# Kernel optimization log

Hardware: AMD Instinct MI355X
Metric: run time of the kernel (lower is better)

Reference implementation:

```python
import jax, jax.numpy as jnp
import numpy as np

COMMA_ID = 1010   # BERT wordpiece id for ','
H, NH, HD = 768, 8, 96
B, S = 64, 512
NSEG = 17         # 16 commas per row -> 17 segments
EPS = 1e-5


def setup_inputs() -> dict:
    key = jax.random.key(0)
    ks = jax.random.split(key, 16)
    text_hs = jax.random.normal(ks[0], (B, S, H), jnp.float32)
    cols_hs = jax.random.normal(ks[1], (B, S, H), jnp.float32)
    ids = jax.random.randint(ks[2], (B, S), 0, 30522)
    ids = jnp.where(ids == COMMA_ID, COMMA_ID + 1, ids)  # avoid accidental commas
    comma_pos = jnp.arange(16, 257, 16)                  # 16 commas per row
    ids = ids.at[:, comma_pos].set(COMMA_ID)
    sc = 0.02
    wq = jax.random.normal(ks[3], (H, H), jnp.float32) * sc
    wk = jax.random.normal(ks[4], (H, H), jnp.float32) * sc
    wv = jax.random.normal(ks[5], (H, H), jnp.float32) * sc
    bq = jnp.zeros((H,), jnp.float32)
    bk = jnp.zeros((H,), jnp.float32)
    bv = jnp.zeros((H,), jnp.float32)
    wo = jax.random.normal(ks[6], (H, H), jnp.float32) * sc
    bo = jnp.zeros((H,), jnp.float32)
    gamma = jnp.ones((H,), jnp.float32)
    beta = jnp.zeros((H,), jnp.float32)
    w_out = jax.random.normal(ks[7], (1, H), jnp.float32) * sc
    b_out = jnp.zeros((1,), jnp.float32)
    return dict(text_hs=text_hs, cols_hs=cols_hs, wq=wq, wk=wk, wv=wv,
                bq=bq, bk=bk, bv=bv, wo=wo, bo=bo, gamma=gamma, beta=beta,
                w_out=w_out, b_out=b_out, columns_input_ids=ids, n_segments=NSEG)


def _forward(text_hs, cols_hs, wq, wk, wv, bq, bk, bv, wo, bo,
             gamma, beta, w_out, b_out, columns_input_ids, n_segments):
    t = text_hs[:, 1:, :]   # drop first token, as in forward()  [B, L, H]
    c = cols_hs[:, 1:, :]
    L = t.shape[1]
    # --- nn.MultiheadAttention(query=cols, key=value=text), batch_first ---
    q = c @ wq.T + bq
    k = t @ wk.T + bk
    v = t @ wv.T + bv
    split = lambda x: x.reshape(x.shape[0], -1, NH, HD).transpose(0, 2, 1, 3)
    scores = jnp.einsum('bhqd,bhkd->bhqk', split(q), split(k)) / np.sqrt(HD).astype(np.float32)
    attn = jax.nn.softmax(scores, axis=-1)
    ctx = jnp.einsum('bhqk,bhkd->bhqd', attn, split(v))
    ctx = ctx.transpose(0, 2, 1, 3).reshape(c.shape[0], L, H)
    attn_out = ctx @ wo.T + bo
    # --- BatchNorm1d over channels (training-mode batch stats) ---
    xt = attn_out.transpose(0, 2, 1)            # [B, H, L]
    mu = xt.mean(axis=(0, 2), keepdims=True)
    var = xt.var(axis=(0, 2), keepdims=True)     # biased, as torch BN normalization
    xn = (xt - mu) / jnp.sqrt(var + EPS) * gamma[None, :, None] + beta[None, :, None]
    cross_out = c + xn.transpose(0, 2, 1)       # residual add
    fv = (cross_out @ w_out.T + b_out).squeeze(-1)   # [B, L] scores per token
    # --- compose_outputs: mean-pool comma-delimited ragged spans ---
    is_comma = columns_input_ids[:, :L] == COMMA_ID
    seg = jnp.cumsum(is_comma.astype(jnp.int32), axis=1) - is_comma.astype(jnp.int32)
    mask = (jnp.arange(L)[None, :] >= 1) & (~is_comma)    # slice_start=1, commas excluded
    oh = ((seg[:, :, None] == jnp.arange(n_segments)[None, None, :])
          & mask[:, :, None]).astype(fv.dtype)            # [B, L, J]
    sums = jnp.einsum('blj,bl->bj', oh, fv)
    cnt = oh.sum(axis=1)
    return sums / jnp.maximum(cnt, 1.0)                   # [B, n_segments]


def reference(text_hs, cols_hs, wq, wk, wv, bq, bk, bv, wo, bo,
              gamma, beta, w_out, b_out, columns_input_ids, n_segments):
    return _forward(text_hs, cols_hs, wq, wk, wv, bq, bk, bv, wo, bo,
                    gamma, beta, w_out, b_out, columns_input_ids, n_segments)
```

## Files before the change

kernel.cpp:

```cpp
#include <hip/hip_runtime.h>
#include <hip/hip_bf16.h>

#define COMMA_IDC 1010
#define NHEAD 8
#define Ll 511
#define Mrows 32704
#define NSEG 17

typedef __attribute__((ext_vector_type(8))) short bf16x8;
typedef __attribute__((ext_vector_type(4))) float f32x4;
typedef unsigned short u16;
typedef unsigned int u32;
typedef unsigned long long u64;

__device__ __forceinline__ u16 f2b(float f) {
  __hip_bfloat16 h = __float2bfloat16(f);
  return *reinterpret_cast<u16*>(&h);
}
__device__ __forceinline__ float b2f(u16 u) {
  u32 x = ((u32)u) << 16;
  return __builtin_bit_cast(float, x);
}

__device__ __forceinline__ void gld_lds16(const void* g, void* l) {
  __builtin_amdgcn_global_load_lds(
      (const __attribute__((address_space(1))) void*)(u64)g,
      (__attribute__((address_space(3))) void*)(u32)(u64)l,
      16, 0, 0);
}

#define MFMA16(a, b, c) __builtin_amdgcn_mfma_f32_16x16x32_bf16(a, b, c, 0, 0, 0)
#define LGKM0 do { asm volatile("s_waitcnt lgkmcnt(0)" ::: "memory"); __builtin_amdgcn_sched_barrier(0); } while (0)
#define VMC(n) asm volatile("s_waitcnt vmcnt(" #n ")" ::: "memory")

__global__ void conv_sliced2(const float4* __restrict__ s0, const float4* __restrict__ s1,
                             ushort4* __restrict__ d0, ushort4* __restrict__ d1) {
  const float4* src = blockIdx.z ? s1 : s0;
  ushort4* dst = blockIdx.z ? d1 : d0;
  int b = blockIdx.y;
  int idx = blockIdx.x * 256 + threadIdx.x;
  if (idx >= Ll * 192) return;
  int l = idx / 192, c = idx - l * 192;
  float4 v = src[(b * 512 + l + 1) * 192 + c];
  ushort4 o; o.x = f2b(v.x); o.y = f2b(v.y); o.z = f2b(v.z); o.w = f2b(v.w);
  dst[(b * Ll + l) * 192 + c] = o;
}

__global__ void conv_w(const float4* __restrict__ wq, const float4* __restrict__ wk,
                       const float4* __restrict__ wv, const float4* __restrict__ wo,
                       ushort4* __restrict__ wqkvb, ushort4* __restrict__ wob) {
  int i = blockIdx.x * 256 + threadIdx.x;
  int seg = i / 147456, off = i - seg * 147456;
  const float4* s = (seg == 0) ? wq : ((seg == 1) ? wk : ((seg == 2) ? wv : wo));
  ushort4* d = (seg == 3) ? wob : (wqkvb + seg * 147456);
  float4 v = s[off];
  ushort4 o; o.x = f2b(v.x); o.y = f2b(v.y); o.z = f2b(v.z); o.w = f2b(v.w);
  d[off] = o;
}

__global__ void zero_kernel(float* p, int n) {
  int i = blockIdx.x * 256 + threadIdx.x;
  if (i < n) p[i] = 0.f;
}

#define LDA8(db, i, kk) (*(const bf16x8*)(sMem + (db) + ((i) * 32 + wr * 16 + fr) * 64 + ((((kk) * 4 + fq) ^ xm) << 3)))
#define LDW8(db, j, kk) (*(const bf16x8*)(sMem + (db) + 16384 + ((j) * 64 + wc * 16 + fr) * 64 + ((((kk) * 4 + fq) ^ xm) << 3)))

template<int NTILES, int NOUT, int QNT, bool DO_STATS>
__global__ __launch_bounds__(512, 2) void gemm256(
    const u16* __restrict__ A0, const u16* __restrict__ A1, const u16* __restrict__ W,
    const float* __restrict__ b0, const float* __restrict__ b1, const float* __restrict__ b2,
    u16* __restrict__ outp, float* __restrict__ ssum, float* __restrict__ ssq)
{
  __shared__ __align__(16) u16 sMem[65536];
  const int tid = threadIdx.x;
  const int lane = tid & 63, wid = tid >> 6;
  const int fr = lane & 15, fq = lane >> 4;
  const int wr = wid >> 2, wc = wid & 3;
  const int xm = fr & 7;

  int fid = blockIdx.x;
  int xcd = fid & 7, w = fid >> 3;
  int mrow = xcd * 16 + w / NTILES;
  int ncol = w - (w / NTILES) * NTILES;
  const int m0 = mrow * 256, n0 = ncol * 256;
  const u16* __restrict__ A = (ncol < QNT) ? A0 : A1;

  const int rS = tid >> 3;
  const int cS = (tid & 7) ^ (rS & 7);
  const u16* gA0 = A + (u64)(m0 + rS) * 768 + cS * 8;
  const u16* gW0 = W + (u64)(n0 + rS) * 768 + cS * 8;
  const u32 st0 = tid * 8;

  auto stALO = [&](u32 db, int kb) {
    gld_lds16(gA0 + kb, sMem + db + st0);
    gld_lds16(gA0 + kb + 49152, sMem + db + st0 + 4096);
  };
  auto stWLO = [&](u32 db, int kb) {
    gld_lds16(gW0 + kb, sMem + db + 16384 + st0);
    gld_lds16(gW0 + kb + 49152, sMem + db + 16384 + st0 + 4096);
  };
  auto stAHI = [&](u32 db, int kb) {
    gld_lds16(gA0 + kb + 98304, sMem + db + 8192 + st0);
    gld_lds16(gA0 + kb + 147456, sMem + db + 8192 + st0 + 4096);
  };
  auto stWHI = [&](u32 db, int kb) {
    gld_lds16(gW0 + kb + 98304, sMem + db + 24576 + st0);
    gld_lds16(gW0 + kb + 147456, sMem + db + 24576 + st0 + 4096);
  };

  f32x4 acc[8][4] = {};
  bf16x8 af[4][2], wl[2][2], wh[2][2];

  stALO(0, 0); stWLO(0, 0); stAHI(0, 0); stWHI(0, 0);
  VMC(4);
  __builtin_amdgcn_s_barrier();

#pragma unroll 1
  for (int kt = 0; kt < 11; ++kt) {
    const u32 db = (u32)(kt & 1) * 32768;
    const u32 nb = db ^ 32768u;
    const int kb1 = (kt + 1) * 64;

#pragma unroll
    for (int i = 0; i < 4; i++) { af[i][0] = LDA8(db, i, 0); af[i][1] = LDA8(db, i, 1); }
#pragma unroll
    for (int j = 0; j < 2; j++) { wl[j][0] = LDW8(db, j, 0); wl[j][1] = LDW8(db, j, 1); }
    stALO(nb, kb1);
    __builtin_amdgcn_s_barrier();
    LGKM0;
    __builtin_amdgcn_s_setprio(1);
#pragma unroll
    for (int i = 0; i < 4; i++)
#pragma unroll
      for (int j = 0; j < 2; j++) {
        acc[i][j] = MFMA16(af[i][0], wl[j][0], acc[i][j]);
        acc[i][j] = MFMA16(af[i][1], wl[j][1], acc[i][j]);
      }
    __builtin_amdgcn_s_setprio(0);
    VMC(4);
    __builtin_amdgcn_s_barrier();

#pragma unroll
    for (int i = 0; i < 4; i++) { af[i][0] = LDA8(db, i + 4, 0); af[i][1] = LDA8(db, i + 4, 1); }
    stWLO(nb, kb1);
    __builtin_amdgcn_s_barrier();
    LGKM0;
    __builtin_amdgcn_s_setprio(1);
#pragma unroll
    for (int i = 0; i < 4; i++)
#pragma unroll
      for (int j = 0; j < 2; j++) {
        acc[i + 4][j] = MFMA16(af[i][0], wl[j][0], acc[i + 4][j]);
        acc[i + 4][j] = MFMA16(af[i][1], wl[j][1], acc[i + 4][j]);
      }
    __builtin_amdgcn_s_setprio(0);
    VMC(4);
    __builtin_amdgcn_s_barrier();

#pragma unroll
    for (int j = 0; j < 2; j++) { wh[j][0] = LDW8(db, j + 2, 0); wh[j][1] = LDW8(db, j + 2, 1); }
    stAHI(nb, kb1);
    __builtin_amdgcn_s_barrier();
    LGKM0;
    __builtin_amdgcn_s_setprio(1);
#pragma unroll
    for (int i = 0; i < 4; i++)
#pragma unroll
      for (int j = 0; j < 2; j++) {
        acc[i + 4][j + 2] = MFMA16(af[i][0], wh[j][0], acc[i + 4][j + 2]);
        acc[i + 4][j + 2] = MFMA16(af[i][1], wh[j][1], acc[i + 4][j + 2]);
      }
    __builtin_amdgcn_s_setprio(0);
    __builtin_amdgcn_s_barrier();

#pragma unroll
    for (int i = 0; i < 4; i++) { af[i][0] = LDA8(db, i, 0); af[i][1] = LDA8(db, i, 1); }
    stWHI(nb, kb1);
    __builtin_amdgcn_s_barrier();
    LGKM0;
    __builtin_amdgcn_s_setprio(1);
#pragma unroll
    for (int i = 0; i < 4; i++)
#pragma unroll
      for (int j = 0; j < 2; j++) {
        acc[i][j + 2] = MFMA16(af[i][0], wh[j][0], acc[i][j + 2]);
        acc[i][j + 2] = MFMA16(af[i][1], wh[j][1], acc[i][j + 2]);
      }
    __builtin_amdgcn_s_setprio(0);
    VMC(4);
    __builtin_amdgcn_s_barrier();
  }

  {
    const u32 db = 32768u;
#pragma unroll
    for (int i = 0; i < 4; i++) { af[i][0] = LDA8(db, i, 0); af[i][1] = LDA8(db, i, 1); }
#pragma unroll
    for (int j = 0; j < 2; j++) { wl[j][0] = LDW8(db, j, 0); wl[j][1] = LDW8(db, j, 1); }
    __builtin_amdgcn_s_barrier();
    LGKM0;
#pragma unroll
    for (int i = 0; i < 4; i++)
#pragma unroll
      for (int j = 0; j < 2; j++) {
        acc[i][j] = MFMA16(af[i][0], wl[j][0], acc[i][j]);
        acc[i][j] = MFMA16(af[i][1], wl[j][1], acc[i][j]);
      }
    VMC(2);
    __builtin_amdgcn_s_barrier();
#pragma unroll
    for (int i = 0; i < 4; i++) { af[i][0] = LDA8(db, i + 4, 0); af[i][1] = LDA8(db, i + 4, 1); }
    __builtin_amdgcn_s_barrier();
    LGKM0;
#pragma unroll
    for (int i = 0; i < 4; i++)
#pragma unroll
      for (int j = 0; j < 2; j++) {
        acc[i + 4][j] = MFMA16(af[i][0], wl[j][0], acc[i + 4][j]);
        acc[i + 4][j] = MFMA16(af[i][1], wl[j][1], acc[i + 4][j]);
      }
    VMC(0);
    __builtin_amdgcn_s_barrier();
#pragma unroll
    for (int j = 0; j < 2; j++) { wh[j][0] = LDW8(db, j + 2, 0); wh[j][1] = LDW8(db, j + 2, 1); }
    LGKM0;
#pragma unroll
    for (int i = 0; i < 4; i++)
#pragma unroll
      for (int j = 0; j < 2; j++) {
        acc[i + 4][j + 2] = MFMA16(af[i][0], wh[j][0], acc[i + 4][j + 2]);
        acc[i + 4][j + 2] = MFMA16(af[i][1], wh[j][1], acc[i + 4][j + 2]);
      }
#pragma unroll
    for (int i = 0; i < 4; i++) { af[i][0] = LDA8(db, i, 0); af[i][1] = LDA8(db, i, 1); }
    LGKM0;
#pragma unroll
    for (int i = 0; i < 4; i++)
#pragma unroll
      for (int j = 0; j < 2; j++) {
        acc[i][j + 2] = MFMA16(af[i][0], wh[j][0], acc[i][j + 2]);
        acc[i][j + 2] = MFMA16(af[i][1], wh[j][1], acc[i][j + 2]);
      }
  }

  const float* bp = (n0 < 768) ? b0 : ((n0 < 1536) ? b1 : b2);
  const int bcol = n0 % 768;
  float bj[4];
#pragma unroll
  for (int j = 0; j < 4; j++) bj[j] = bp[bcol + j * 64 + wc * 16 + fr];

  if constexpr (DO_STATS) {
#pragma unroll
    for (int j = 0; j < 4; j++) {
      float s = 0.f, q = 0.f;
#pragma unroll
      for (int i = 0; i < 8; i++)
#pragma unroll
        for (int r = 0; r < 4; r++) {
          int m = m0 + i * 32 + wr * 16 + fq * 4 + r;
          float v = acc[i][j][r] + bj[j];
          if (m < Mrows) { s += v; q += v * v; }
        }
      s += __shfl_xor(s, 16, 64); s += __shfl_xor(s, 32, 64);
      q += __shfl_xor(q, 16, 64); q += __shfl_xor(q, 32, 64);
      if (fq == 0) {
        int col = n0 + j * 64 + wc * 16 + fr;
        atomicAdd(&ssum[col], s);
        atomicAdd(&ssq[col], q);
      }
    }
  }

#pragma unroll
  for (int h = 0; h < 2; h++) {
    __syncthreads();
#pragma unroll
    for (int i2 = 0; i2 < 4; i2++) {
      int i = h * 4 + i2;
#pragma unroll
      for (int j = 0; j < 4; j++)
#pragma unroll
        for (int r = 0; r < 4; r++)
          sMem[(i2 * 32 + wr * 16 + fq * 4 + r) * 264 + j * 64 + wc * 16 + fr] =
              f2b(acc[i][j][r] + bj[j]);
    }
    __syncthreads();
#pragma unroll
    for (int it = 0; it < 8; it++) {
      int chunk = tid + it * 512;
      int lr = chunk >> 5, ch = chunk & 31;
      *(bf16x8*)(outp + (u64)(m0 + h * 128 + lr) * NOUT + n0 + ch * 8) =
          *(const bf16x8*)(sMem + lr * 264 + ch * 8);
    }
  }
}

__global__ __launch_bounds__(256) void vtrans(const u16* __restrict__ QKV, u16* __restrict__ VT) {
  __shared__ __align__(16) u16 sT[128 * 128];
  int bh = blockIdx.y;
  int b = bh >> 3, h = bh & 7;
  int l0 = blockIdx.x * 128;
  u16* outp = VT + (u64)bh * 96 * 512;
  int t = threadIdx.x;
#pragma unroll
  for (int k = 0; k < 6; k++) {
    int c = t + k * 256;
    int l = c / 12, ch = c - l * 12;
    int lc = l0 + l; if (lc > 510) lc = 510;
    bf16x8 v = *(const bf16x8*)(QKV + (u64)(b * 511 + lc) * 2304 + 1536 + h * 96 + ch * 8);
    int chunk = l * 16 + (ch ^ ((l >> 3) & 7));
    *(bf16x8*)(sT + chunk * 8) = v;
  }
  __syncthreads();
#pragma unroll
  for (int k = 0; k < 6; k++) {
    int c = t + k * 256;
    int d = c >> 4, lch = c & 15;
    u16 vals[8];
#pragma unroll
    for (int k2 = 0; k2 < 8; k2++) {
      int r = lch * 8 + k2;
      int idx = r * 128 + (((d >> 3) ^ (lch & 7)) << 3) + (d & 7);
      vals[k2] = sT[idx];
    }
    bf16x8 o;
#pragma unroll
    for (int k2 = 0; k2 < 8; k2++) o[k2] = (short)vals[k2];
    *(bf16x8*)(outp + (u64)d * 512 + l0 + lch * 8) = o;
  }
}

#define PST 68
__global__ __launch_bounds__(256) void attn_kernel(
    const u16* __restrict__ QKV, const u16* __restrict__ VT, u16* __restrict__ ctxb)
{
  __shared__ __align__(16) u16 sK[64 * 96];
  __shared__ __align__(16) u16 sV[96 * 64];
  __shared__ __align__(16) u16 sP[4][16 * PST];
  const int tid = threadIdx.x, lane = tid & 63, wid = tid >> 6;
  int fid = blockIdx.x;
  int xcd = fid & 7, slot = (fid >> 3) & 3, grp = fid >> 5;
  int bh = grp * 8 + xcd;
  int b = bh >> 3, h = bh & 7;
  int q0 = slot * 128;
  const int fr = lane & 15, fq = lane >> 4;
  const u64 mb = (u64)(b * 511);
  const u64 hbV = (u64)bh * 96 * 512;

  bf16x8 qf[2][3];
#pragma unroll
  for (int sub = 0; sub < 2; sub++) {
    int qr = q0 + wid * 32 + sub * 16 + fr; if (qr > 510) qr = 510;
#pragma unroll
    for (int ks = 0; ks < 3; ks++)
      qf[sub][ks] = *(const bf16x8*)(QKV + (mb + qr) * 2304 + h * 96 + ks * 32 + fq * 8);
  }

  f32x4 ctx[2][6] = {};
  f32x4 sumP[2] = {};

  int kRow[3]; u32 kOffG[3], vOffG[3];
  u16 *kDst[3], *vDst[3];
#pragma unroll
  for (int k = 0; k < 3; k++) {
    int c = wid * 64 + lane + k * 256;
    int r = c / 12, p = c - r * 12;
    int s = p - (r % 12); if (s < 0) s += 12;
    kRow[k] = r;
    kOffG[k] = 768 + h * 96 + s * 8;
    kDst[k] = sK + (u32)(wid * 64 + k * 256) * 8;
    int d = c >> 3, pv = c & 7;
    int sv = pv ^ (d & 7);
    vOffG[k] = (u32)(d * 512 + sv * 8);
    vDst[k] = sV + (u32)(wid * 64 + k * 256) * 8;
  }

  const float cs = 0.10206207261596575f;
  u16* pw = &sP[wid][0];

  for (int kv0 = 0; kv0 < 511; kv0 += 64) {
    __syncthreads();
#pragma unroll
    for (int k = 0; k < 3; k++) {
      int row = kv0 + kRow[k]; if (row > 510) row = 510;
      gld_lds16(QKV + (mb + row) * 2304 + kOffG[k], kDst[k]);
    }
#pragma unroll
    for (int k = 0; k < 3; k++)
      gld_lds16(VT + hbV + vOffG[k] + kv0, vDst[k]);
    __syncthreads();

    bf16x8 kf[4][3];
#pragma unroll
    for (int kv16 = 0; kv16 < 4; kv16++) {
      int r = kv16 * 16 + fr;
      int rm = r % 12;
#pragma unroll
      for (int ks = 0; ks < 3; ks++) {
        int sidx = ks * 4 + fq + rm; if (sidx >= 12) sidx -= 12;
        kf[kv16][ks] = *(const bf16x8*)(sK + (r * 12 + sidx) * 8);
      }
    }

#pragma unroll
    for (int sub = 0; sub < 2; sub++) {
      f32x4 s[4] = {};
#pragma unroll
      for (int kv16 = 0; kv16 < 4; kv16++)
#pragma unroll
        for (int ks = 0; ks < 3; ks++)
          s[kv16] = MFMA16(qf[sub][ks], kf[kv16][ks], s[kv16]);

#pragma unroll
      for (int kv16 = 0; kv16 < 4; kv16++) {
        bool ok = (kv0 + kv16 * 16 + fr) < Ll;
#pragma unroll
        for (int r = 0; r < 4; r++) {
          float e = __expf(s[kv16][r] * cs);
          e = ok ? e : 0.f;
          sumP[sub][r] += e;
          pw[(fq * 4 + r) * PST + kv16 * 16 + fr] = f2b(e);
        }
      }
      bf16x8 pf0 = *(const bf16x8*)(pw + fr * PST + fq * 8);
      bf16x8 pf1 = *(const bf16x8*)(pw + fr * PST + 32 + fq * 8);
#pragma unroll
      for (int df = 0; df < 6; df++) {
        int row = df * 16 + fr;
        int xv = fr & 7;
        bf16x8 vf0 = *(const bf16x8*)(sV + row * 64 + ((fq ^ xv) << 3));
        bf16x8 vf1 = *(const bf16x8*)(sV + row * 64 + (((4 + fq) ^ xv) << 3));
        ctx[sub][df] = MFMA16(pf0, vf0, ctx[sub][df]);
        ctx[sub][df] = MFMA16(pf1, vf1, ctx[sub][df]);
      }
    }
  }

#pragma unroll
  for (int sub = 0; sub < 2; sub++) {
    float inv[4];
#pragma unroll
    for (int r = 0; r < 4; r++) {
      float s = sumP[sub][r];
      s += __shfl_xor(s, 1, 64);
      s += __shfl_xor(s, 2, 64);
      s += __shfl_xor(s, 4, 64);
      s += __shfl_xor(s, 8, 64);
      inv[r] = 1.f / s;
    }
#pragma unroll
    for (int df = 0; df < 6; df++) {
#pragma unroll
      for (int r = 0; r < 4; r++) {
        int q = q0 + wid * 32 + sub * 16 + fq * 4 + r;
        if (q < Ll)
          ctxb[(u64)(b * Ll + q) * 768 + h * 96 + df * 16 + fr] = f2b(ctx[sub][df][r] * inv[r]);
      }
    }
  }
}

__global__ __launch_bounds__(256) void derived_kernel(
    const float* __restrict__ ssum, const float* __restrict__ ssq,
    const float* __restrict__ w_out, const float* __restrict__ b_out,
    const float* __restrict__ gamma, const float* __restrict__ beta,
    float* __restrict__ weff, float* __restrict__ consts)
{
  __shared__ float red[256];
  int t = threadIdx.x;
  float acc = 0.f;
  const float invN = 1.f / 32704.f;
#pragma unroll
  for (int i = 0; i < 3; i++) {
    int hh = t + i * 256;
    float mu = ssum[hh] * invN;
    float var = ssq[hh] * invN - mu * mu;
    float rstd = 1.f / sqrtf(var + 1e-5f);
    float we = w_out[hh] * gamma[hh] * rstd;
    weff[hh] = we;
    acc += w_out[hh] * beta[hh] - we * mu;
  }
  red[t] = acc; __syncthreads();
  for (int s = 128; s > 0; s >>= 1) { if (t < s) red[t] += red[t + s]; __syncthreads(); }
  if (t == 0) consts[0] = b_out[0] + red[0];
}

__global__ __launch_bounds__(256) void fv_kernel(
    const u16* __restrict__ ao, const u16* __restrict__ cb,
    const float* __restrict__ w_out, const float* __restrict__ weff,
    const float* __restrict__ consts, float* __restrict__ fv)
{
  int lane = threadIdx.x & 63, wid = threadIdx.x >> 6;
  int m = blockIdx.x * 4 + wid;
  if (m >= Mrows) return;
  const u16* ap = ao + (u64)m * 768;
  const u16* cp = cb + (u64)m * 768;
  float acc = 0.f;
#pragma unroll
  for (int i = 0; i < 12; i++) {
    int hh = lane + i * 64;
    acc += b2f(ap[hh]) * weff[hh] + b2f(cp[hh]) * w_out[hh];
  }
#pragma unroll
  for (int off = 1; off < 64; off <<= 1) acc += __shfl_xor(acc, off, 64);
  if (lane == 0) fv[m] = acc + consts[0];
}

__global__ __launch_bounds__(64) void seg_kernel(
    const float* __restrict__ fv, const int* __restrict__ ids, float* __restrict__ out)
{
  __shared__ float ssum[NSEG];
  __shared__ int scnt[NSEG];
  int lane = threadIdx.x;
  int b = blockIdx.x;
  if (lane < NSEG) { ssum[lane] = 0.f; scnt[lane] = 0; }
  __syncthreads();
  int carry = 0;
  for (int it = 0; it < 8; it++) {
    int l = it * 64 + lane;
    bool active = l < Ll;
    int id = active ? ids[b * 512 + l] : 0;
    bool comma = active && (id == COMMA_IDC);
    u64 cmask = __ballot(comma);
    int seg = carry + __popcll(cmask & ((1ull << lane) - 1ull));
    bool valid = active && (l >= 1) && !comma;
    if (valid && seg < NSEG) {
      atomicAdd(&ssum[seg], fv[b * Ll + l]);
      atomicAdd(&scnt[seg], 1);
    }
    carry += __popcll(cmask);
  }
  __syncthreads();
  if (lane < NSEG) {
    float c = (float)scnt[lane];
    out[b * NSEG + lane] = ssum[lane] / fmaxf(c, 1.f);
  }
}

extern "C" void kernel_launch(void* const* d_in, const int* in_sizes, int n_in,
                              void* d_out, int out_size, void* d_ws, size_t ws_size,
                              hipStream_t stream)
{
  const float* text  = (const float*)d_in[0];
  const float* cols  = (const float*)d_in[1];
  const float* wq    = (const float*)d_in[2];
  const float* wk    = (const float*)d_in[3];
  const float* wvp   = (const float*)d_in[4];
  const float* bq    = (const float*)d_in[5];
  const float* bk    = (const float*)d_in[6];
  const float* bv    = (const float*)d_in[7];
  const float* wo    = (const float*)d_in[8];
  const float* bo    = (const float*)d_in[9];
  const float* gamma = (const float*)d_in[10];
  const float* beta  = (const float*)d_in[11];
  const float* w_out = (const float*)d_in[12];
  const float* b_out = (const float*)d_in[13];
  const int*   ids   = (const int*)d_in[14];
  float* out = (float*)d_out;

  char* ws = (char*)d_ws;
  u16* cb    = (u16*)(ws + 0ull);
  u16* tb    = (u16*)(ws + 50331648ull);
  u16* wqkvb = (u16*)(ws + 100663296ull);
  u16* wob   = (u16*)(ws + 104202240ull);
  u16* QKVb  = (u16*)(ws + 105381888ull);
  u16* ctxb  = (u16*)(ws + 256376832ull);
  u16* VTb   = tb;
  u16* aob   = QKVb;
  float* ssum   = (float*)(ws + 105381888ull + 50331648ull);
  float* ssq    = ssum + 768;
  float* weff   = ssum + 1536;
  float* consts = ssum + 2304;
  float* fv     = (float*)((char*)ssum + 16384ull);

  conv_sliced2<<<dim3(384, 64, 2), 256, 0, stream>>>(
      (const float4*)cols, (const float4*)text, (ushort4*)cb, (ushort4*)tb);
  conv_w<<<2304, 256, 0, stream>>>(
      (const float4*)wq, (const float4*)wk, (const float4*)wvp, (const float4*)wo,
      (ushort4*)wqkvb, (ushort4*)wob);

  gemm256<9, 2304, 3, false><<<1152, 512, 0, stream>>>(
      cb, tb, wqkvb, bq, bk, bv, QKVb, nullptr, nullptr);
  vtrans<<<dim3(4, 512), 256, 0, stream>>>(QKVb, VTb);
  attn_kernel<<<2048, 256, 0, stream>>>(QKVb, VTb, ctxb);

  zero_kernel<<<6, 256, 0, stream>>>(ssum, 1536);
  gemm256<3, 768, 99, true><<<384, 512, 0, stream>>>(
      ctxb, ctxb, wob, bo, bo, bo, aob, ssum, ssq);
  derived_kernel<<<1, 256, 0, stream>>>(ssum, ssq, w_out, b_out, gamma, beta, weff, consts);
  fv_kernel<<<8176, 256, 0, stream>>>(aob, cb, w_out, weff, consts, fv);
  seg_kernel<<<64, 64, 0, stream>>>(fv, ids, out);
}
```

Measured before the change: 412.7 us.

## Shrink GEMM tiles to 128x128 and fuse V transpose into QKV GEMM epilogue

```diff
diff --git a/kernel.cpp b/kernel.cpp
--- a/kernel.cpp
+++ b/kernel.cpp
@@ -64,26 +64,27 @@
 }
 
 #define LDA8(db, i, kk) (*(const bf16x8*)(sMem + (db) + ((i) * 32 + wr * 16 + fr) * 64 + ((((kk) * 4 + fq) ^ xm) << 3)))
-#define LDW8(db, j, kk) (*(const bf16x8*)(sMem + (db) + 16384 + ((j) * 64 + wc * 16 + fr) * 64 + ((((kk) * 4 + fq) ^ xm) << 3)))
-
-template<int NTILES, int NOUT, int QNT, bool DO_STATS>
-__global__ __launch_bounds__(512, 2) void gemm256(
+#define LDW8(db, j, kk) (*(const bf16x8*)(sMem + (db) + 8192 + ((j) * 32 + wc * 16 + fr) * 64 + ((((kk) * 4 + fq) ^ xm) << 3)))
+
+template<int NTILES, int NOUT, int QNT, int VSTART, bool DO_STATS>
+__global__ __launch_bounds__(256, 4) void gemm128(
     const u16* __restrict__ A0, const u16* __restrict__ A1, const u16* __restrict__ W,
     const float* __restrict__ b0, const float* __restrict__ b1, const float* __restrict__ b2,
-    u16* __restrict__ outp, float* __restrict__ ssum, float* __restrict__ ssq)
+    u16* __restrict__ outp, u16* __restrict__ VT,
+    float* __restrict__ ssum, float* __restrict__ ssq)
 {
-  __shared__ __align__(16) u16 sMem[65536];
+  __shared__ __align__(16) u16 sMem[32768];
   const int tid = threadIdx.x;
   const int lane = tid & 63, wid = tid >> 6;
   const int fr = lane & 15, fq = lane >> 4;
-  const int wr = wid >> 2, wc = wid & 3;
+  const int wr = wid >> 1, wc = wid & 1;
   const int xm = fr & 7;
 
   int fid = blockIdx.x;
-  int xcd = fid & 7, w = fid >> 3;
-  int mrow = xcd * 16 + w / NTILES;
-  int ncol = w - (w / NTILES) * NTILES;
-  const int m0 = mrow * 256, n0 = ncol * 256;
+  int xcd = fid & 7, t = fid >> 3;
+  int mrow = xcd * 32 + t / NTILES;
+  int ncol = t - (t / NTILES) * NTILES;
+  const int m0 = mrow * 128, n0 = ncol * 128;
   const u16* __restrict__ A = (ncol < QNT) ? A0 : A1;
 
   const int rS = tid >> 3;
@@ -94,23 +95,23 @@
 
   auto stALO = [&](u32 db, int kb) {
     gld_lds16(gA0 + kb, sMem + db + st0);
-    gld_lds16(gA0 + kb + 49152, sMem + db + st0 + 4096);
+    gld_lds16(gA0 + kb + 24576, sMem + db + st0 + 2048);
+  };
+  auto stAHI = [&](u32 db, int kb) {
+    gld_lds16(gA0 + kb + 49152, sMem + db + 4096 + st0);
+    gld_lds16(gA0 + kb + 73728, sMem + db + 4096 + st0 + 2048);
   };
   auto stWLO = [&](u32 db, int kb) {
-    gld_lds16(gW0 + kb, sMem + db + 16384 + st0);
-    gld_lds16(gW0 + kb + 49152, sMem + db + 16384 + st0 + 4096);
-  };
-  auto stAHI = [&](u32 db, int kb) {
-    gld_lds16(gA0 + kb + 98304, sMem + db + 8192 + st0);
-    gld_lds16(gA0 + kb + 147456, sMem + db + 8192 + st0 + 4096);
+    gld_lds16(gW0 + kb, sMem + db + 8192 + st0);
+    gld_lds16(gW0 + kb + 24576, sMem + db + 8192 + st0 + 2048);
   };
   auto stWHI = [&](u32 db, int kb) {
-    gld_lds16(gW0 + kb + 98304, sMem + db + 24576 + st0);
-    gld_lds16(gW0 + kb + 147456, sMem + db + 24576 + st0 + 4096);
+    gld_lds16(gW0 + kb + 49152, sMem + db + 12288 + st0);
+    gld_lds16(gW0 + kb + 73728, sMem + db + 12288 + st0 + 2048);
   };
 
-  f32x4 acc[8][4] = {};
-  bf16x8 af[4][2], wl[2][2], wh[2][2];
+  f32x4 acc[4][4] = {};
+  bf16x8 af[2][2], wl[2][2];
 
   stALO(0, 0); stWLO(0, 0); stAHI(0, 0); stWHI(0, 0);
   VMC(4);
@@ -118,12 +119,12 @@
 
 #pragma unroll 1
   for (int kt = 0; kt < 11; ++kt) {
-    const u32 db = (u32)(kt & 1) * 32768;
-    const u32 nb = db ^ 32768u;
+    const u32 db = (u32)(kt & 1) * 16384;
+    const u32 nb = db ^ 16384u;
     const int kb1 = (kt + 1) * 64;
 
 #pragma unroll
-    for (int i = 0; i < 4; i++) { af[i][0] = LDA8(db, i, 0); af[i][1] = LDA8(db, i, 1); }
+    for (int i = 0; i < 2; i++) { af[i][0] = LDA8(db, i, 0); af[i][1] = LDA8(db, i, 1); }
 #pragma unroll
     for (int j = 0; j < 2; j++) { wl[j][0] = LDW8(db, j, 0); wl[j][1] = LDW8(db, j, 1); }
     stALO(nb, kb1);
@@ -131,7 +132,7 @@
     LGKM0;
     __builtin_amdgcn_s_setprio(1);
 #pragma unroll
-    for (int i = 0; i < 4; i++)
+    for (int i = 0; i < 2; i++)
 #pragma unroll
       for (int j = 0; j < 2; j++) {
         acc[i][j] = MFMA16(af[i][0], wl[j][0], acc[i][j]);
@@ -142,50 +143,50 @@
     __builtin_amdgcn_s_barrier();
 
 #pragma unroll
-    for (int i = 0; i < 4; i++) { af[i][0] = LDA8(db, i + 4, 0); af[i][1] = LDA8(db, i + 4, 1); }
+    for (int i = 0; i < 2; i++) { af[i][0] = LDA8(db, i + 2, 0); af[i][1] = LDA8(db, i + 2, 1); }
     stWLO(nb, kb1);
     __builtin_amdgcn_s_barrier();
     LGKM0;
     __builtin_amdgcn_s_setprio(1);
 #pragma unroll
-    for (int i = 0; i < 4; i++)
-#pragma unroll
-      for (int j = 0; j < 2; j++) {
-        acc[i + 4][j] = MFMA16(af[i][0], wl[j][0], acc[i + 4][j]);
-        acc[i + 4][j] = MFMA16(af[i][1], wl[j][1], acc[i + 4][j]);
+    for (int i = 0; i < 2; i++)
+#pragma unroll
+      for (int j = 0; j < 2; j++) {
+        acc[i + 2][j] = MFMA16(af[i][0], wl[j][0], acc[i + 2][j]);
+        acc[i + 2][j] = MFMA16(af[i][1], wl[j][1], acc[i + 2][j]);
       }
     __builtin_amdgcn_s_setprio(0);
     VMC(4);
     __builtin_amdgcn_s_barrier();
 
 #pragma unroll
-    for (int j = 0; j < 2; j++) { wh[j][0] = LDW8(db, j + 2, 0); wh[j][1] = LDW8(db, j + 2, 1); }
+    for (int j = 0; j < 2; j++) { wl[j][0] = LDW8(db, j + 2, 0); wl[j][1] = LDW8(db, j + 2, 1); }
     stAHI(nb, kb1);
     __builtin_amdgcn_s_barrier();
     LGKM0;
     __builtin_amdgcn_s_setprio(1);
 #pragma unroll
-    for (int i = 0; i < 4; i++)
-#pragma unroll
-      for (int j = 0; j < 2; j++) {
-        acc[i + 4][j + 2] = MFMA16(af[i][0], wh[j][0], acc[i + 4][j + 2]);
-        acc[i + 4][j + 2] = MFMA16(af[i][1], wh[j][1], acc[i + 4][j + 2]);
+    for (int i = 0; i < 2; i++)
+#pragma unroll
+      for (int j = 0; j < 2; j++) {
+        acc[i + 2][j + 2] = MFMA16(af[i][0], wl[j][0], acc[i + 2][j + 2]);
+        acc[i + 2][j + 2] = MFMA16(af[i][1], wl[j][1], acc[i + 2][j + 2]);
       }
     __builtin_amdgcn_s_setprio(0);
     __builtin_amdgcn_s_barrier();
 
 #pragma unroll
-    for (int i = 0; i < 4; i++) { af[i][0] = LDA8(db, i, 0); af[i][1] = LDA8(db, i, 1); }
+    for (int i = 0; i < 2; i++) { af[i][0] = LDA8(db, i, 0); af[i][1] = LDA8(db, i, 1); }
     stWHI(nb, kb1);
     __builtin_amdgcn_s_barrier();
     LGKM0;
     __builtin_amdgcn_s_setprio(1);
 #pragma unroll
-    for (int i = 0; i < 4; i++)
-#pragma unroll
-      for (int j = 0; j < 2; j++) {
-        acc[i][j + 2] = MFMA16(af[i][0], wh[j][0], acc[i][j + 2]);
-        acc[i][j + 2] = MFMA16(af[i][1], wh[j][1], acc[i][j + 2]);
+    for (int i = 0; i < 2; i++)
+#pragma unroll
+      for (int j = 0; j < 2; j++) {
+        acc[i][j + 2] = MFMA16(af[i][0], wl[j][0], acc[i][j + 2]);
+        acc[i][j + 2] = MFMA16(af[i][1], wl[j][1], acc[i][j + 2]);
       }
     __builtin_amdgcn_s_setprio(0);
     VMC(4);
@@ -193,15 +194,15 @@
   }
 
   {
-    const u32 db = 32768u;
-#pragma unroll
-    for (int i = 0; i < 4; i++) { af[i][0] = LDA8(db, i, 0); af[i][1] = LDA8(db, i, 1); }
+    const u32 db = 16384u;
+#pragma unroll
+    for (int i = 0; i < 2; i++) { af[i][0] = LDA8(db, i, 0); af[i][1] = LDA8(db, i, 1); }
 #pragma unroll
     for (int j = 0; j < 2; j++) { wl[j][0] = LDW8(db, j, 0); wl[j][1] = LDW8(db, j, 1); }
     __builtin_amdgcn_s_barrier();
     LGKM0;
 #pragma unroll
-    for (int i = 0; i < 4; i++)
+    for (int i = 0; i < 2; i++)
 #pragma unroll
       for (int j = 0; j < 2; j++) {
         acc[i][j] = MFMA16(af[i][0], wl[j][0], acc[i][j]);
@@ -210,37 +211,37 @@
     VMC(2);
     __builtin_amdgcn_s_barrier();
 #pragma unroll
-    for (int i = 0; i < 4; i++) { af[i][0] = LDA8(db, i + 4, 0); af[i][1] = LDA8(db, i + 4, 1); }
-    __builtin_amdgcn_s_barrier();
-    LGKM0;
-#pragma unroll
-    for (int i = 0; i < 4; i++)
-#pragma unroll
-      for (int j = 0; j < 2; j++) {
-        acc[i + 4][j] = MFMA16(af[i][0], wl[j][0], acc[i + 4][j]);
-        acc[i + 4][j] = MFMA16(af[i][1], wl[j][1], acc[i + 4][j]);
+    for (int i = 0; i < 2; i++) { af[i][0] = LDA8(db, i + 2, 0); af[i][1] = LDA8(db, i + 2, 1); }
+    __builtin_amdgcn_s_barrier();
+    LGKM0;
+#pragma unroll
+    for (int i = 0; i < 2; i++)
+#pragma unroll
+      for (int j = 0; j < 2; j++) {
+        acc[i + 2][j] = MFMA16(af[i][0], wl[j][0], acc[i + 2][j]);
+        acc[i + 2][j] = MFMA16(af[i][1], wl[j][1], acc[i + 2][j]);
       }
     VMC(0);
     __builtin_amdgcn_s_barrier();
 #pragma unroll
-    for (int j = 0; j < 2; j++) { wh[j][0] = LDW8(db, j + 2, 0); wh[j][1] = LDW8(db, j + 2, 1); }
-    LGKM0;
-#pragma unroll
-    for (int i = 0; i < 4; i++)
-#pragma unroll
-      for (int j = 0; j < 2; j++) {
-        acc[i + 4][j + 2] = MFMA16(af[i][0], wh[j][0], acc[i + 4][j + 2]);
-        acc[i + 4][j + 2] = MFMA16(af[i][1], wh[j][1], acc[i + 4][j + 2]);
-      }
-#pragma unroll
-    for (int i = 0; i < 4; i++) { af[i][0] = LDA8(db, i, 0); af[i][1] = LDA8(db, i, 1); }
-    LGKM0;
-#pragma unroll
-    for (int i = 0; i < 4; i++)
-#pragma unroll
-      for (int j = 0; j < 2; j++) {
-        acc[i][j + 2] = MFMA16(af[i][0], wh[j][0], acc[i][j + 2]);
-        acc[i][j + 2] = MFMA16(af[i][1], wh[j][1], acc[i][j + 2]);
+    for (int j = 0; j < 2; j++) { wl[j][0] = LDW8(db, j + 2, 0); wl[j][1] = LDW8(db, j + 2, 1); }
+    LGKM0;
+#pragma unroll
+    for (int i = 0; i < 2; i++)
+#pragma unroll
+      for (int j = 0; j < 2; j++) {
+        acc[i + 2][j + 2] = MFMA16(af[i][0], wl[j][0], acc[i + 2][j + 2]);
+        acc[i + 2][j + 2] = MFMA16(af[i][1], wl[j][1], acc[i + 2][j + 2]);
+      }
+#pragma unroll
+    for (int i = 0; i < 2; i++) { af[i][0] = LDA8(db, i, 0); af[i][1] = LDA8(db, i, 1); }
+    LGKM0;
+#pragma unroll
+    for (int i = 0; i < 2; i++)
+#pragma unroll
+      for (int j = 0; j < 2; j++) {
+        acc[i][j + 2] = MFMA16(af[i][0], wl[j][0], acc[i][j + 2]);
+        acc[i][j + 2] = MFMA16(af[i][1], wl[j][1], acc[i][j + 2]);
       }
   }
 
@@ -248,14 +249,14 @@
   const int bcol = n0 % 768;
   float bj[4];
 #pragma unroll
-  for (int j = 0; j < 4; j++) bj[j] = bp[bcol + j * 64 + wc * 16 + fr];
+  for (int j = 0; j < 4; j++) bj[j] = bp[bcol + j * 32 + wc * 16 + fr];
 
   if constexpr (DO_STATS) {
 #pragma unroll
     for (int j = 0; j < 4; j++) {
       float s = 0.f, q = 0.f;
 #pragma unroll
-      for (int i = 0; i < 8; i++)
+      for (int i = 0; i < 4; i++)
 #pragma unroll
         for (int r = 0; r < 4; r++) {
           int m = m0 + i * 32 + wr * 16 + fq * 4 + r;
@@ -265,75 +266,73 @@
       s += __shfl_xor(s, 16, 64); s += __shfl_xor(s, 32, 64);
       q += __shfl_xor(q, 16, 64); q += __shfl_xor(q, 32, 64);
       if (fq == 0) {
-        int col = n0 + j * 64 + wc * 16 + fr;
+        int col = n0 + j * 32 + wc * 16 + fr;
         atomicAdd(&ssum[col], s);
         atomicAdd(&ssq[col], q);
       }
     }
   }
 
-#pragma unroll
-  for (int h = 0; h < 2; h++) {
+  if (ncol >= VSTART) {
     __syncthreads();
 #pragma unroll
-    for (int i2 = 0; i2 < 4; i2++) {
-      int i = h * 4 + i2;
+    for (int i = 0; i < 4; i++)
 #pragma unroll
       for (int j = 0; j < 4; j++)
 #pragma unroll
         for (int r = 0; r < 4; r++)
-          sMem[(i2 * 32 + wr * 16 + fq * 4 + r) * 264 + j * 64 + wc * 16 + fr] =
+          sMem[(j * 32 + wc * 16 + fr) * 136 + i * 32 + wr * 16 + fq * 4 + r] =
               f2b(acc[i][j][r] + bj[j]);
-    }
     __syncthreads();
 #pragma unroll
     for (int it = 0; it < 8; it++) {
-      int chunk = tid + it * 512;
-      int lr = chunk >> 5, ch = chunk & 31;
-      *(bf16x8*)(outp + (u64)(m0 + h * 128 + lr) * NOUT + n0 + ch * 8) =
-          *(const bf16x8*)(sMem + lr * 264 + ch * 8);
-    }
-  }
-}
-
-__global__ __launch_bounds__(256) void vtrans(const u16* __restrict__ QKV, u16* __restrict__ VT) {
-  __shared__ __align__(16) u16 sT[128 * 128];
-  int bh = blockIdx.y;
-  int b = bh >> 3, h = bh & 7;
-  int l0 = blockIdx.x * 128;
-  u16* outp = VT + (u64)bh * 96 * 512;
-  int t = threadIdx.x;
-#pragma unroll
-  for (int k = 0; k < 6; k++) {
-    int c = t + k * 256;
-    int l = c / 12, ch = c - l * 12;
-    int lc = l0 + l; if (lc > 510) lc = 510;
-    bf16x8 v = *(const bf16x8*)(QKV + (u64)(b * 511 + lc) * 2304 + 1536 + h * 96 + ch * 8);
-    int chunk = l * 16 + (ch ^ ((l >> 3) & 7));
-    *(bf16x8*)(sT + chunk * 8) = v;
-  }
-  __syncthreads();
-#pragma unroll
-  for (int k = 0; k < 6; k++) {
-    int c = t + k * 256;
-    int d = c >> 4, lch = c & 15;
-    u16 vals[8];
-#pragma unroll
-    for (int k2 = 0; k2 < 8; k2++) {
-      int r = lch * 8 + k2;
-      int idx = r * 128 + (((d >> 3) ^ (lch & 7)) << 3) + (d & 7);
-      vals[k2] = sT[idx];
-    }
-    bf16x8 o;
-#pragma unroll
-    for (int k2 = 0; k2 < 8; k2++) o[k2] = (short)vals[k2];
-    *(bf16x8*)(outp + (u64)d * 512 + l0 + lch * 8) = o;
+      int chunk = tid + it * 256;
+      int dcol = chunk >> 4, lch = chunk & 15;
+      bf16x8 v = *(const bf16x8*)(sMem + dcol * 136 + lch * 8);
+      int nv = n0 + dcol - 1536;
+      int hh = nv / 96, dd = nv - hh * 96;
+      int mstart = m0 + lch * 8;
+      int bb = mstart / 511, be = (mstart + 7) / 511;
+      if (bb == be && mstart + 7 < Mrows) {
+        int l = mstart - bb * 511;
+        *(bf16x8*)(VT + ((u64)(bb * 8 + hh) * 96 + dd) * 512 + l) = v;
+      } else {
+#pragma unroll
+        for (int k = 0; k < 8; k++) {
+          int m = mstart + k;
+          if (m < Mrows) {
+            int b2i = m / 511, l = m - b2i * 511;
+            VT[((u64)(b2i * 8 + hh) * 96 + dd) * 512 + l] = (u16)v[k];
+          }
+        }
+      }
+    }
+  } else {
+    __syncthreads();
+#pragma unroll
+    for (int i = 0; i < 4; i++)
+#pragma unroll
+      for (int j = 0; j < 4; j++)
+#pragma unroll
+        for (int r = 0; r < 4; r++)
+          sMem[(i * 32 + wr * 16 + fq * 4 + r) * 136 + j * 32 + wc * 16 + fr] =
+              f2b(acc[i][j][r] + bj[j]);
+    __syncthreads();
+#pragma unroll
+    for (int it = 0; it < 8; it++) {
+      int chunk = tid + it * 256;
+      int lr = chunk >> 4, ch = chunk & 15;
+      int m = m0 + lr;
+      if (m < Mrows)
+        *(bf16x8*)(outp + (u64)m * NOUT + n0 + ch * 8) =
+            *(const bf16x8*)(sMem + lr * 136 + ch * 8);
+    }
   }
 }
 
 #define PST 68
 __global__ __launch_bounds__(256) void attn_kernel(
-    const u16* __restrict__ QKV, const u16* __restrict__ VT, u16* __restrict__ ctxb)
+    const u16* __restrict__ QK, const u16* __restrict__ VT, u16* __restrict__ ctxb)
 {
   __shared__ __align__(16) u16 sK[64 * 96];
   __shared__ __align__(16) u16 sV[96 * 64];
@@ -354,7 +353,7 @@
     int qr = q0 + wid * 32 + sub * 16 + fr; if (qr > 510) qr = 510;
 #pragma unroll
     for (int ks = 0; ks < 3; ks++)
-      qf[sub][ks] = *(const bf16x8*)(QKV + (mb + qr) * 2304 + h * 96 + ks * 32 + fq * 8);
+      qf[sub][ks] = *(const bf16x8*)(QK + (mb + qr) * 1536 + h * 96 + ks * 32 + fq * 8);
   }
 
   f32x4 ctx[2][6] = {};
@@ -384,7 +383,7 @@
 #pragma unroll
     for (int k = 0; k < 3; k++) {
       int row = kv0 + kRow[k]; if (row > 510) row = 510;
-      gld_lds16(QKV + (mb + row) * 2304 + kOffG[k], kDst[k]);
+      gld_lds16(QK + (mb + row) * 1536 + kOffG[k], kDst[k]);
     }
 #pragma unroll
     for (int k = 0; k < 3; k++)
@@ -564,15 +563,15 @@
   u16* tb    = (u16*)(ws + 50331648ull);
   u16* wqkvb = (u16*)(ws + 100663296ull);
   u16* wob   = (u16*)(ws + 104202240ull);
-  u16* QKVb  = (u16*)(ws + 105381888ull);
+  u16* QKb   = (u16*)(ws + 105381888ull);
+  u16* VTb   = (u16*)(ws + 206045184ull);
   u16* ctxb  = (u16*)(ws + 256376832ull);
-  u16* VTb   = tb;
-  u16* aob   = QKVb;
-  float* ssum   = (float*)(ws + 105381888ull + 50331648ull);
+  u16* aob   = QKb;
+  float* ssum   = (float*)VTb;
   float* ssq    = ssum + 768;
   float* weff   = ssum + 1536;
   float* consts = ssum + 2304;
-  float* fv     = (float*)((char*)ssum + 16384ull);
+  float* fv     = (float*)((char*)VTb + 16384ull);
 
   conv_sliced2<<<dim3(384, 64, 2), 256, 0, stream>>>(
       (const float4*)cols, (const float4*)text, (ushort4*)cb, (ushort4*)tb);
@@ -580,14 +579,13 @@
       (const float4*)wq, (const float4*)wk, (const float4*)wvp, (const float4*)wo,
       (ushort4*)wqkvb, (ushort4*)wob);
 
-  gemm256<9, 2304, 3, false><<<1152, 512, 0, stream>>>(
-      cb, tb, wqkvb, bq, bk, bv, QKVb, nullptr, nullptr);
-  vtrans<<<dim3(4, 512), 256, 0, stream>>>(QKVb, VTb);
-  attn_kernel<<<2048, 256, 0, stream>>>(QKVb, VTb, ctxb);
+  gemm128<18, 1536, 6, 12, false><<<4608, 256, 0, stream>>>(
+      cb, tb, wqkvb, bq, bk, bv, QKb, VTb, nullptr, nullptr);
+  attn_kernel<<<2048, 256, 0, stream>>>(QKb, VTb, ctxb);
 
   zero_kernel<<<6, 256, 0, stream>>>(ssum, 1536);
-  gemm256<3, 768, 99, true><<<384, 512, 0, stream>>>(
-      ctxb, ctxb, wob, bo, bo, bo, aob, ssum, ssq);
+  gemm128<6, 768, 99, 99, true><<<1536, 256, 0, stream>>>(
+      ctxb, ctxb, wob, bo, bo, bo, aob, nullptr, ssum, ssq);
   derived_kernel<<<1, 256, 0, stream>>>(ssum, ssq, w_out, b_out, gamma, beta, weff, consts);
   fv_kernel<<<8176, 256, 0, stream>>>(aob, cb, w_out, weff, consts, fv);
   seg_kernel<<<64, 64, 0, stream>>>(fv, ids, out);
```

Result: slower. 432.6 us (+4.8%).
